# Kernel tuning notes

Hardware: AMD Instinct MI355X
Metric: run time of the kernel (lower is better)

Reference implementation:

```python
import jax, jax.numpy as jnp
import numpy as np

N_NODES = 2048
N_EDGES = 32768
NEG_SLOPE = 0.01  # torch F.leaky_relu default used in DGL GAT tutorial


def gat_layer(h, W, a, src, dst):
    """Multi-head GAT layer (DGL tutorial math), concat merge.
    h: [N, F_in], W: [H, F_in, D], a: [H, 2D], src/dst: [E].
    Returns [N, H*D].
    """
    n = h.shape[0]
    D = W.shape[2]
    z = jnp.einsum('ni,hio->nho', h, W)                      # [N,H,D]
    a_src, a_dst = a[:, :D], a[:, D:]
    s_src = jnp.einsum('nhd,hd->nh', z, a_src)               # [N,H]
    s_dst = jnp.einsum('nhd,hd->nh', z, a_dst)               # [N,H]
    e = jax.nn.leaky_relu(s_src[src] + s_dst[dst], NEG_SLOPE)  # [E,H]
    # softmax over incoming edges per destination node
    e_max = jax.ops.segment_max(e, dst, num_segments=n)      # [N,H]
    ex = jnp.exp(e - e_max[dst])                             # [E,H]
    denom = jax.ops.segment_sum(ex, dst, num_segments=n)     # [N,H]
    alpha = ex / denom[dst]                                  # [E,H]
    msg = alpha[:, :, None] * z[src]                         # [E,H,D]
    out = jax.ops.segment_sum(msg, dst, num_segments=n)      # [N,H,D]
    return out.reshape(n, -1)


def setup_inputs() -> dict:
    key = jax.random.key(0)
    ks = jax.random.split(key, 12)

    def w(k, h, i, o):
        return jax.random.normal(k, (h, i, o), jnp.float32) / np.float32(np.sqrt(i))

    def av(k, h, o):
        return jax.random.normal(k, (h, 2 * o), jnp.float32) / np.float32(np.sqrt(2 * o))

    feat = jax.random.normal(ks[0], (N_NODES, 512), jnp.float32)
    W1 = w(ks[1], 16, 512, 512);   a1 = av(ks[2], 16, 512)
    W2 = w(ks[3], 16, 8192, 512);  a2 = av(ks[4], 16, 512)
    W3 = w(ks[5], 16, 8192, 512);  a3 = av(ks[6], 16, 512)
    W4 = w(ks[7], 1, 8192, 512);   a4 = av(ks[8], 1, 512)
    src = jax.random.randint(ks[9], (N_EDGES,), 0, N_NODES, jnp.int32)
    # guarantee every node has at least one incoming edge (no empty softmax)
    dst_rand = jax.random.randint(ks[10], (N_EDGES - N_NODES,), 0, N_NODES, jnp.int32)
    dst = jnp.concatenate([jnp.arange(N_NODES, dtype=jnp.int32), dst_rand])
    return dict(feat=feat, W1=W1, a1=a1, W2=W2, a2=a2, W3=W3, a3=a3,
                W4=W4, a4=a4, src=src, dst=dst)


def reference(feat, W1, a1, W2, a2, W3, a3, W4, a4, src, dst):
    x = gat_layer(feat, W1, a1, src, dst)   # [N, 8192]
    x = gat_layer(x, W2, a2, src, dst)      # [N, 8192]
    x = gat_layer(x, W3, a3, src, dst)      # [N, 8192]
    x = gat_layer(x, W4, a4, src, dst)      # [N, 512]
    return x
```

## Files before the change

### kernel.cpp

```cpp
#include <hip/hip_runtime.h>
#include <hip/hip_bf16.h>
#include <stdint.h>

#define N_NODES 2048
#define N_EDGES 32768

using short8  = __attribute__((ext_vector_type(8))) short;
using floatx4 = __attribute__((ext_vector_type(4))) float;

__device__ __forceinline__ unsigned short f2bf(float f) {
  unsigned u = __float_as_uint(f);
  unsigned r = (u + 0x7fffu + ((u >> 16) & 1u)) >> 16;
  return (unsigned short)r;
}
__device__ __forceinline__ float wave_sum(float v) {
  #pragma unroll
  for (int o = 32; o > 0; o >>= 1) v += __shfl_xor(v, o);
  return v;
}
__device__ __forceinline__ float wave_max(float v) {
  #pragma unroll
  for (int o = 32; o > 0; o >>= 1) v = fmaxf(v, __shfl_xor(v, o));
  return v;
}

__global__ __launch_bounds__(256) void cast_feat(
    const float* __restrict__ in, unsigned short* __restrict__ out, int n4)
{
  int i = blockIdx.x * 256 + threadIdx.x;
  if (i < n4) {
    float4 v = ((const float4*)in)[i];
    ushort4 o;
    o.x = f2bf(v.x); o.y = f2bf(v.y); o.z = f2bf(v.z); o.w = f2bf(v.w);
    ((ushort4*)out)[i] = o;
  }
}

__global__ __launch_bounds__(256) void transpose_w(
    const float* __restrict__ W, unsigned short* __restrict__ Wt, int Fin)
{
  __shared__ unsigned short tile[64][68];
  const int h  = blockIdx.z;
  const int k0 = blockIdx.x * 64;
  const int d0 = blockIdx.y * 64;
  const int t  = threadIdx.x;
  const float*    Wh  = W  + (size_t)h * Fin * 512;
  unsigned short* Wth = Wt + (size_t)h * 512 * Fin;

  const int dl = (t & 15) * 4;
  const int kr = t >> 4;
  #pragma unroll
  for (int p = 0; p < 4; ++p) {
    int k = kr + p * 16;
    float4 v = *(const float4*)(Wh + (size_t)(k0 + k) * 512 + d0 + dl);
    ushort4 b;
    b.x = f2bf(v.x); b.y = f2bf(v.y); b.z = f2bf(v.z); b.w = f2bf(v.w);
    *(ushort4*)&tile[k][dl] = b;
  }
  __syncthreads();
  const int kl = (t & 15) * 4;
  const int dr = t >> 4;
  #pragma unroll
  for (int p = 0; p < 4; ++p) {
    int d = dr + p * 16;
    ushort4 v;
    v.x = tile[kl + 0][d];
    v.y = tile[kl + 1][d];
    v.z = tile[kl + 2][d];
    v.w = tile[kl + 3][d];
    *(ushort4*)(Wth + (size_t)(d0 + d) * Fin + k0 + kl) = v;
  }
}

__global__ __launch_bounds__(256) void gemm_bt(
    const unsigned short* __restrict__ A,
    const unsigned short* __restrict__ Bt,
    float* __restrict__ C, int K, int HD, int h0, int klen)
{
  __shared__ unsigned short As[128 * 32];
  __shared__ unsigned short Bs[128 * 32];
  const int tid  = threadIdx.x;
  const int w    = tid >> 6;
  const int lane = tid & 63;
  const int mt   = blockIdx.x;
  const int nt   = blockIdx.y;
  const int hloc = nt >> 2;
  const int nloc = (nt & 3) << 7;
  const int kstart = blockIdx.z * klen;

  const unsigned short* Ab = A  + (size_t)mt * 128 * K;
  const unsigned short* Bb = Bt + (size_t)hloc * 512 * K + (size_t)nloc * K;

  const int srow = lane >> 2;
  const int scol = (lane & 3) << 3;
  const unsigned short* ga = Ab + (size_t)(w * 32 + srow) * K + scol + kstart;
  const unsigned short* gb = Bb + (size_t)(w * 32 + srow) * K + scol + kstart;

  floatx4 acc[4][4];
  #pragma unroll
  for (int i = 0; i < 4; ++i)
    #pragma unroll
    for (int j = 0; j < 4; ++j)
      acc[i][j] = (floatx4){0.f, 0.f, 0.f, 0.f};

  const int quad = lane >> 4;
  const int l16  = lane & 15;
  const int wm   = (w >> 1) << 6;
  const int wn   = (w & 1) << 6;

  for (int kb = 0; kb < klen; kb += 32) {
    __builtin_amdgcn_global_load_lds(
        (const __attribute__((address_space(1))) void*)ga,
        (__attribute__((address_space(3))) void*)&As[w * 1024], 16, 0, 0);
    __builtin_amdgcn_global_load_lds(
        (const __attribute__((address_space(1))) void*)(ga + (size_t)16 * K),
        (__attribute__((address_space(3))) void*)&As[w * 1024 + 512], 16, 0, 0);
    __builtin_amdgcn_global_load_lds(
        (const __attribute__((address_space(1))) void*)gb,
        (__attribute__((address_space(3))) void*)&Bs[w * 1024], 16, 0, 0);
    __builtin_amdgcn_global_load_lds(
        (const __attribute__((address_space(1))) void*)(gb + (size_t)16 * K),
        (__attribute__((address_space(3))) void*)&Bs[w * 1024 + 512], 16, 0, 0);
    ga += 32; gb += 32;
    __syncthreads();

    short8 af[4], bfr[4];
    #pragma unroll
    for (int mi = 0; mi < 4; ++mi)
      af[mi] = *(const short8*)&As[(wm + mi * 16 + l16) * 32 + quad * 8];
    #pragma unroll
    for (int ni = 0; ni < 4; ++ni)
      bfr[ni] = *(const short8*)&Bs[(wn + ni * 16 + l16) * 32 + quad * 8];
    #pragma unroll
    for (int mi = 0; mi < 4; ++mi)
      #pragma unroll
      for (int ni = 0; ni < 4; ++ni)
        acc[mi][ni] = __builtin_amdgcn_mfma_f32_16x16x32_bf16(
            af[mi], bfr[ni], acc[mi][ni], 0, 0, 0);
    __syncthreads();
  }

  float* Cb = C + (size_t)(mt * 128) * HD + (h0 + hloc) * 512 + nloc;
  if (gridDim.z > 1) {
    #pragma unroll
    for (int mi = 0; mi < 4; ++mi)
      #pragma unroll
      for (int ni = 0; ni < 4; ++ni)
        #pragma unroll
        for (int r = 0; r < 4; ++r) {
          int row = wm + mi * 16 + quad * 4 + r;
          int col = wn + ni * 16 + l16;
          atomicAdd(&Cb[(size_t)row * HD + col], acc[mi][ni][r]);
        }
  } else {
    #pragma unroll
    for (int mi = 0; mi < 4; ++mi)
      #pragma unroll
      for (int ni = 0; ni < 4; ++ni)
        #pragma unroll
        for (int r = 0; r < 4; ++r) {
          int row = wm + mi * 16 + quad * 4 + r;
          int col = wn + ni * 16 + l16;
          Cb[(size_t)row * HD + col] = acc[mi][ni][r];
        }
  }
}

__global__ __launch_bounds__(64) void sdot_kernel(
    const float* __restrict__ z, const float* __restrict__ a,
    float* __restrict__ ssrc, float* __restrict__ sdst, int H)
{
  const int idx  = blockIdx.x;
  const int n    = idx / H;
  const int h    = idx % H;
  const int lane = threadIdx.x;
  const float4* zr = (const float4*)(z + (size_t)n * H * 512 + h * 512 + lane * 8);
  float4 z0 = zr[0], z1 = zr[1];
  const float4* as = (const float4*)(a + (size_t)h * 1024 + lane * 8);
  const float4* ad = (const float4*)(a + (size_t)h * 1024 + 512 + lane * 8);
  float4 a0 = as[0], a1 = as[1];
  float4 b0 = ad[0], b1 = ad[1];
  float s1 = z0.x*a0.x + z0.y*a0.y + z0.z*a0.z + z0.w*a0.w
           + z1.x*a1.x + z1.y*a1.y + z1.z*a1.z + z1.w*a1.w;
  float s2 = z0.x*b0.x + z0.y*b0.y + z0.z*b0.z + z0.w*b0.w
           + z1.x*b1.x + z1.y*b1.y + z1.z*b1.z + z1.w*b1.w;
  s1 = wave_sum(s1);
  s2 = wave_sum(s2);
  if (lane == 0) { ssrc[idx] = s1; sdst[idx] = s2; }
}

__global__ void count_k(const int* __restrict__ dst, int* __restrict__ cnt) {
  int e = blockIdx.x * 256 + threadIdx.x;
  if (e < N_EDGES) atomicAdd(&cnt[dst[e]], 1);
}

__global__ __launch_bounds__(256) void scan_k(
    const int* __restrict__ cnt, int* __restrict__ offs, int* __restrict__ cur)
{
  __shared__ int part[256];
  int t = threadIdx.x;
  int loc[8]; int s = 0;
  #pragma unroll
  for (int j = 0; j < 8; ++j) { loc[j] = s; s += cnt[t * 8 + j]; }
  part[t] = s;
  __syncthreads();
  for (int d = 1; d < 256; d <<= 1) {
    int v = (t >= d) ? part[t - d] : 0;
    __syncthreads();
    part[t] += v;
    __syncthreads();
  }
  int base = (t == 0) ? 0 : part[t - 1];
  #pragma unroll
  for (int j = 0; j < 8; ++j) {
    int o = base + loc[j];
    offs[t * 8 + j] = o;
    cur[t * 8 + j]  = o;
  }
  if (t == 255) offs[2048] = part[255];
}

__global__ void scatter_k(const int* __restrict__ dst, const int* __restrict__ srcv,
                          int* __restrict__ cur, int* __restrict__ esrc) {
  int e = blockIdx.x * 256 + threadIdx.x;
  if (e < N_EDGES) {
    int p = atomicAdd(&cur[dst[e]], 1);
    esrc[p] = srcv[e];
  }
}

__global__ __launch_bounds__(64) void attn_agg(
    const float* __restrict__ z, const float* __restrict__ ssrc,
    const float* __restrict__ sdst, const int* __restrict__ offs,
    const int* __restrict__ esrc, unsigned short* __restrict__ outb,
    float* __restrict__ outf, int H)
{
  const int n = blockIdx.x, h = blockIdx.y, lane = threadIdx.x;
  const int s0 = offs[n], s1 = offs[n + 1];
  const float sd = sdst[n * H + h];

  float m = -3e38f;
  for (int i = s0 + lane; i < s1; i += 64) {
    float s = ssrc[esrc[i] * H + h] + sd;
    s = (s > 0.f) ? s : s * 0.01f;
    m = fmaxf(m, s);
  }
  m = wave_max(m);

  float den = 0.f;
  for (int i = s0 + lane; i < s1; i += 64) {
    float s = ssrc[esrc[i] * H + h] + sd;
    s = (s > 0.f) ? s : s * 0.01f;
    den += __expf(s - m);
  }
  den = wave_sum(den);
  const float inv = 1.f / den;

  float acc[8] = {0.f, 0.f, 0.f, 0.f, 0.f, 0.f, 0.f, 0.f};
  const float* zb = z + (size_t)h * 512 + lane * 8;
  for (int i = s0; i < s1; ++i) {
    int se = esrc[i];
    float s = ssrc[se * H + h] + sd;
    s = (s > 0.f) ? s : s * 0.01f;
    float alpha = __expf(s - m) * inv;
    const float4* zr = (const float4*)(zb + (size_t)se * H * 512);
    float4 q0 = zr[0], q1 = zr[1];
    acc[0] += alpha * q0.x; acc[1] += alpha * q0.y;
    acc[2] += alpha * q0.z; acc[3] += alpha * q0.w;
    acc[4] += alpha * q1.x; acc[5] += alpha * q1.y;
    acc[6] += alpha * q1.z; acc[7] += alpha * q1.w;
  }

  const size_t base = (size_t)n * H * 512 + h * 512 + lane * 8;
  if (outf) {
    float4 o0 = {acc[0], acc[1], acc[2], acc[3]};
    float4 o1 = {acc[4], acc[5], acc[6], acc[7]};
    *(float4*)(outf + base)     = o0;
    *(float4*)(outf + base + 4) = o1;
  } else {
    uint4 pk;
    pk.x = (unsigned)f2bf(acc[0]) | ((unsigned)f2bf(acc[1]) << 16);
    pk.y = (unsigned)f2bf(acc[2]) | ((unsigned)f2bf(acc[3]) << 16);
    pk.z = (unsigned)f2bf(acc[4]) | ((unsigned)f2bf(acc[5]) << 16);
    pk.w = (unsigned)f2bf(acc[6]) | ((unsigned)f2bf(acc[7]) << 16);
    *(uint4*)(outb + base) = pk;
  }
}

extern "C" void kernel_launch(void* const* d_in, const int* in_sizes, int n_in,
                              void* d_out, int out_size, void* d_ws, size_t ws_size,
                              hipStream_t stream)
{
  (void)in_sizes; (void)n_in; (void)out_size;
  const float* feat = (const float*)d_in[0];
  const float* W1   = (const float*)d_in[1];
  const float* a1   = (const float*)d_in[2];
  const float* W2   = (const float*)d_in[3];
  const float* a2   = (const float*)d_in[4];
  const float* W3   = (const float*)d_in[5];
  const float* a3   = (const float*)d_in[6];
  const float* W4   = (const float*)d_in[7];
  const float* a4   = (const float*)d_in[8];
  const int* src = (const int*)d_in[9];
  const int* dst = (const int*)d_in[10];
  float* out = (float*)d_out;

  const size_t WT16 = (size_t)16 * 512 * 8192 * 2;
  const size_t WT8  = WT16 / 2;
  const size_t ZSZ  = (size_t)N_NODES * 16 * 512 * 4;
  const size_t XSZ  = (size_t)N_NODES * 8192 * 2;
  const size_t X0SZ = (size_t)N_NODES * 512 * 2;
  const size_t SMALL = 131072 + 131072 + 8192 + 8448 + 8192 + 131072;
  const size_t NEED16 = WT16 + ZSZ + XSZ + X0SZ + SMALL;

  const int ngroups = (ws_size >= NEED16) ? 1 : 2;
  const size_t wtsz = (ngroups == 1) ? WT16 : WT8;

  char* ws = (char*)d_ws;
  unsigned short* wt = (unsigned short*)ws;
  float* z           = (float*)(ws + wtsz);
  unsigned short* x  = (unsigned short*)(ws + wtsz + ZSZ);
  unsigned short* x0 = (unsigned short*)(ws + wtsz + ZSZ + XSZ);
  char* sm           = ws + wtsz + ZSZ + XSZ + X0SZ;
  float* ssrc        = (float*)(sm);
  float* sdst        = (float*)(sm + 131072);
  int* cnt           = (int*)(sm + 262144);
  int* offs          = (int*)(sm + 270336);
  int* cur           = (int*)(sm + 278784);
  int* esrc          = (int*)(sm + 286976);

  hipMemsetAsync(cnt, 0, N_NODES * sizeof(int), stream);
  count_k<<<N_EDGES / 256, 256, 0, stream>>>(dst, cnt);
  scan_k<<<1, 256, 0, stream>>>(cnt, offs, cur);
  scatter_k<<<N_EDGES / 256, 256, 0, stream>>>(dst, src, cur, esrc);

  cast_feat<<<1024, 256, 0, stream>>>(feat, x0, N_NODES * 512 / 4);

  auto run_gemm = [&](const float* W, const unsigned short* xin,
                      int Fin, int H, int ksplit) {
    const int groups = (H == 16) ? ngroups : 1;
    const int hpg = H / groups;
    for (int g = 0; g < groups; ++g) {
      transpose_w<<<dim3(Fin / 64, 8, hpg), 256, 0, stream>>>(
          W + (size_t)g * hpg * Fin * 512, wt, Fin);
      if (ksplit > 1)
        hipMemsetAsync(z, 0, (size_t)N_NODES * H * 512 * sizeof(float), stream);
      gemm_bt<<<dim3(16, hpg * 4, ksplit), 256, 0, stream>>>(
          xin, wt, z, Fin, H * 512, g * hpg, Fin / ksplit);
    }
  };

  run_gemm(W1, x0, 512, 16, 1);
  sdot_kernel<<<N_NODES * 16, 64, 0, stream>>>(z, a1, ssrc, sdst, 16);
  attn_agg<<<dim3(N_NODES, 16), 64, 0, stream>>>(z, ssrc, sdst, offs, esrc,
                                                 x, nullptr, 16);

  run_gemm(W2, x, 8192, 16, 1);
  sdot_kernel<<<N_NODES * 16, 64, 0, stream>>>(z, a2, ssrc, sdst, 16);
  attn_agg<<<dim3(N_NODES, 16), 64, 0, stream>>>(z, ssrc, sdst, offs, esrc,
                                                 x, nullptr, 16);

  run_gemm(W3, x, 8192, 16, 1);
  sdot_kernel<<<N_NODES * 16, 64, 0, stream>>>(z, a3, ssrc, sdst, 16);
  attn_agg<<<dim3(N_NODES, 16), 64, 0, stream>>>(z, ssrc, sdst, offs, esrc,
                                                 x, nullptr, 16);

  run_gemm(W4, x, 8192, 1, 8);
  sdot_kernel<<<N_NODES, 64, 0, stream>>>(z, a4, ssrc, sdst, 1);
  attn_agg<<<dim3(N_NODES, 1), 64, 0, stream>>>(z, ssrc, sdst, offs, esrc,
                                                nullptr, out, 1);
}
```

Baseline: 1.914 ms.

## Add 256x256-tile bf16 MFMA GEMM with direct global-to-LDS loads for 16-head layers

Adds a new GEMM kernel with 512 threads per block and 256x256 output tiles. It loads operands straight into LDS with global_load_lds through a 4-stage ring buffer, using swizzled layouts and split A/B loads interleaved with MFMA phases and priority hints. This kernel replaces the old 128x128 gemm_bt for layers 1-3, aiming to raise data reuse and overlap memory with compute on the dominant large GEMMs. It also uses a grid remap for locality. Layer 4 keeps the split-K path. The cost is higher register and LDS use, which risks lower occupancy and scheduling fragility.

Measured after the change: 1.540 ms. -19.6%, faster.

```diff
diff --git a/kernel.cpp b/kernel.cpp
--- a/kernel.cpp
+++ b/kernel.cpp
@@ -70,6 +70,149 @@
     v.w = tile[kl + 3][d];
     *(ushort4*)(Wth + (size_t)(d0 + d) * Fin + k0 + kl) = v;
   }
+}
+
+#define GLDS(g, l) __builtin_amdgcn_global_load_lds(                       \
+    (const __attribute__((address_space(1))) void*)(g),                    \
+    (__attribute__((address_space(3))) void*)(l), 16, 0, 0)
+
+__global__ __launch_bounds__(512, 2) void gemm8(
+    const unsigned short* __restrict__ A,
+    const unsigned short* __restrict__ Bt,
+    float* __restrict__ C, int K, int ldc, int colbase)
+{
+  __shared__ __align__(16) unsigned short lds_buf[4][16384];
+
+  const int tid  = threadIdx.x;
+  const int w    = tid >> 6;
+  const int lane = tid & 63;
+  const int l16  = lane & 15;
+  const int quad = lane >> 4;
+  const int warp_m = w >> 2;
+  const int warp_n = w & 3;
+
+  const int nwg = gridDim.x;
+  const int cpx = nwg >> 3;
+  const int wg  = (blockIdx.x & 7) * cpx + (blockIdx.x >> 3);
+  const int mt  = wg & 7;
+  const int nt  = wg >> 3;
+
+  const int NT = K >> 5;
+
+  const int srow = lane >> 2;
+  const int gch  = ((lane & 3) ^ ((lane >> 3) & 3)) * 8;
+  const unsigned short* pa0 = A  + (size_t)(mt * 256 + w * 32 + srow) * K + gch;
+  const unsigned short* pa1 = pa0 + (size_t)16 * K;
+  const unsigned short* pb0 = Bt + (size_t)(nt * 256 + w * 32 + srow) * K + gch;
+  const unsigned short* pb1 = pb0 + (size_t)16 * K;
+
+  const int fA   = (l16 >> 1) & 3;
+  const int cswz = (quad ^ fA) * 8;
+  const int a_off = (warp_m * 128 + l16) * 32 + cswz;
+  const int b_off = 8192 + (warp_n * 64 + l16) * 32 + cswz;
+
+  floatx4 acc[8][4];
+  #pragma unroll
+  for (int i = 0; i < 8; ++i)
+    #pragma unroll
+    for (int j = 0; j < 4; ++j)
+      acc[i][j] = (floatx4){0.f, 0.f, 0.f, 0.f};
+
+  {
+    unsigned short* dA0 = &lds_buf[0][w * 1024];
+    unsigned short* dB0 = &lds_buf[0][8192 + w * 1024];
+    GLDS(pa0, dA0); GLDS(pa1, dA0 + 512);
+    GLDS(pb0, dB0); GLDS(pb1, dB0 + 512);
+    unsigned short* dA1 = &lds_buf[1][w * 1024];
+    unsigned short* dB1 = &lds_buf[1][8192 + w * 1024];
+    GLDS(pa0 + 32, dA1); GLDS(pa1 + 32, dA1 + 512);
+    GLDS(pb0 + 32, dB1); GLDS(pb1 + 32, dB1 + 512);
+  }
+  asm volatile("s_waitcnt vmcnt(4)");
+  __builtin_amdgcn_s_barrier();
+  __builtin_amdgcn_sched_barrier(0);
+
+  const unsigned short* sa0 = pa0 + 64;
+  const unsigned short* sa1 = pa1 + 64;
+  const unsigned short* sb0 = pb0 + 64;
+  const unsigned short* sb1 = pb1 + 64;
+
+  for (int t = 0; t < NT; ++t) {
+    const int s  = t & 3;
+    const int s2 = (t + 2) & 3;
+    const unsigned short* sl  = &lds_buf[s][0];
+    const unsigned short* rdA = sl + a_off;
+    const unsigned short* rdB = sl + b_off;
+    const bool st = (t + 2) < NT;
+
+    short8 af[4], bf4[4];
+    #pragma unroll
+    for (int mi = 0; mi < 4; ++mi)
+      af[mi] = *(const short8*)(rdA + mi * 512);
+    #pragma unroll
+    for (int ni = 0; ni < 4; ++ni)
+      bf4[ni] = *(const short8*)(rdB + ni * 512);
+    if (st) {
+      unsigned short* dA = &lds_buf[s2][w * 1024];
+      GLDS(sa0, dA); GLDS(sa1, dA + 512);
+    }
+    __builtin_amdgcn_sched_barrier(0);
+    __builtin_amdgcn_s_barrier();
+    asm volatile("s_waitcnt lgkmcnt(0)");
+    __builtin_amdgcn_sched_barrier(0);
+    __builtin_amdgcn_s_setprio(1);
+    #pragma unroll
+    for (int mi = 0; mi < 4; ++mi)
+      #pragma unroll
+      for (int ni = 0; ni < 4; ++ni)
+        acc[mi][ni] = __builtin_amdgcn_mfma_f32_16x16x32_bf16(
+            af[mi], bf4[ni], acc[mi][ni], 0, 0, 0);
+    __builtin_amdgcn_s_setprio(0);
+    __builtin_amdgcn_sched_barrier(0);
+    __builtin_amdgcn_s_barrier();
+    __builtin_amdgcn_sched_barrier(0);
+
+    short8 ag[4];
+    #pragma unroll
+    for (int mi = 0; mi < 4; ++mi)
+      ag[mi] = *(const short8*)(rdA + (mi + 4) * 512);
+    if (st) {
+      unsigned short* dB = &lds_buf[s2][8192 + w * 1024];
+      GLDS(sb0, dB); GLDS(sb1, dB + 512);
+    }
+    __builtin_amdgcn_sched_barrier(0);
+    __builtin_amdgcn_s_barrier();
+    asm volatile("s_waitcnt lgkmcnt(0)");
+    __builtin_amdgcn_sched_barrier(0);
+    __builtin_amdgcn_s_setprio(1);
+    #pragma unroll
+    for (int mi = 0; mi < 4; ++mi)
+      #pragma unroll
+      for (int ni = 0; ni < 4; ++ni)
+        acc[mi + 4][ni] = __builtin_amdgcn_mfma_f32_16x16x32_bf16(
+            ag[mi], bf4[ni], acc[mi + 4][ni], 0, 0, 0);
+    __builtin_amdgcn_s_setprio(0);
+    __builtin_amdgcn_sched_barrier(0);
+    if (st) asm volatile("s_waitcnt vmcnt(4)");
+    else    asm volatile("s_waitcnt vmcnt(0)");
+    __builtin_amdgcn_s_barrier();
+    __builtin_amdgcn_sched_barrier(0);
+
+    sa0 += 32; sa1 += 32; sb0 += 32; sb1 += 32;
+  }
+
+  float* Cb = C + (size_t)(mt * 256 + warp_m * 128) * ldc
+                + colbase + nt * 256 + warp_n * 64;
+  #pragma unroll
+  for (int mi = 0; mi < 8; ++mi)
+    #pragma unroll
+    for (int ni = 0; ni < 4; ++ni)
+      #pragma unroll
+      for (int r = 0; r < 4; ++r) {
+        int row = mi * 16 + quad * 4 + r;
+        int col = ni * 16 + l16;
+        Cb[(size_t)row * ldc + col] = acc[mi][ni][r];
+      }
 }
 
 __global__ __launch_bounds__(256) void gemm_bt(
@@ -336,36 +479,36 @@
 
   cast_feat<<<1024, 256, 0, stream>>>(feat, x0, N_NODES * 512 / 4);
 
-  auto run_gemm = [&](const float* W, const unsigned short* xin,
-                      int Fin, int H, int ksplit) {
-    const int groups = (H == 16) ? ngroups : 1;
-    const int hpg = H / groups;
-    for (int g = 0; g < groups; ++g) {
+  auto run_big = [&](const float* W, const unsigned short* xin, int Fin) {
+    const int hpg = 16 / ngroups;
+    for (int g = 0; g < ngroups; ++g) {
       transpose_w<<<dim3(Fin / 64, 8, hpg), 256, 0, stream>>>(
           W + (size_t)g * hpg * Fin * 512, wt, Fin);
-      if (ksplit > 1)
-        hipMemsetAsync(z, 0, (size_t)N_NODES * H * 512 * sizeof(float), stream);
-      gemm_bt<<<dim3(16, hpg * 4, ksplit), 256, 0, stream>>>(
-          xin, wt, z, Fin, H * 512, g * hpg, Fin / ksplit);
+      const int ntn = hpg * 2;
+      gemm8<<<dim3(8 * ntn), 512, 0, stream>>>(
+          xin, wt, z, Fin, 8192, g * hpg * 512);
     }
   };
 
-  run_gemm(W1, x0, 512, 16, 1);
+  transpose_w<<<dim3(8, 8, 16), 256, 0, stream>>>(W1, wt, 512);
+  gemm8<<<dim3(8 * 32), 512, 0, stream>>>(x0, wt, z, 512, 8192, 0);
   sdot_kernel<<<N_NODES * 16, 64, 0, stream>>>(z, a1, ssrc, sdst, 16);
   attn_agg<<<dim3(N_NODES, 16), 64, 0, stream>>>(z, ssrc, sdst, offs, esrc,
                                                  x, nullptr, 16);
 
-  run_gemm(W2, x, 8192, 16, 1);
+  run_big(W2, x, 8192);
   sdot_kernel<<<N_NODES * 16, 64, 0, stream>>>(z, a2, ssrc, sdst, 16);
   attn_agg<<<dim3(N_NODES, 16), 64, 0, stream>>>(z, ssrc, sdst, offs, esrc,
                                                  x, nullptr, 16);
 
-  run_gemm(W3, x, 8192, 16, 1);
+  run_big(W3, x, 8192);
   sdot_kernel<<<N_NODES * 16, 64, 0, stream>>>(z, a3, ssrc, sdst, 16);
   attn_agg<<<dim3(N_NODES, 16), 64, 0, stream>>>(z, ssrc, sdst, offs, esrc,
                                                  x, nullptr, 16);
 
-  run_gemm(W4, x, 8192, 1, 8);
+  transpose_w<<<dim3(128, 8, 1), 256, 0, stream>>>(W4, wt, 8192);
+  hipMemsetAsync(z, 0, (size_t)N_NODES * 512 * sizeof(float), stream);
+  gemm_bt<<<dim3(16, 4, 8), 256, 0, stream>>>(x, wt, z, 8192, 512, 0, 1024);
   sdot_kernel<<<N_NODES, 64, 0, stream>>>(z, a4, ssrc, sdst, 1);
   attn_agg<<<dim3(N_NODES, 1), 64, 0, stream>>>(z, ssrc, sdst, offs, esrc,
                                                 nullptr, out, 1);
```
